# Optimization experiments

Measured on AMD Instinct MI355X. Metric: run time of the kernel, lower is better.

## Reference

```python
import jax, jax.numpy as jnp
import numpy as np

N_QUBITS = 14
N_LAYERS = 3
BATCH = 128


def _apply_1q(state, gate, w, n):
    """Apply a single-qubit gate on wire w (PennyLane wire 0 = most significant bit).
    state: (B, 2**n) complex. gate: (2,2) shared or (B,2,2) batched."""
    L, R = 2 ** w, 2 ** (n - 1 - w)
    s = state.reshape(-1, L, 2, R)
    if gate.ndim == 2:
        s = jnp.einsum('ij,aljr->alir', gate, s)
    else:
        s = jnp.einsum('aij,aljr->alir', gate, s)
    return s.reshape(state.shape)


def _apply_cnot(state, c, t, n):
    """CNOT with control wire c, target wire t on (B, 2**n) state."""
    s = state.reshape((-1,) + (2,) * n)
    ca = 1 + c
    s0 = jax.lax.index_in_dim(s, 0, ca, keepdims=False)
    s1 = jax.lax.index_in_dim(s, 1, ca, keepdims=False)
    # axis of target after removing control axis
    ta = 1 + t if t < c else t
    s1 = jnp.flip(s1, axis=ta)
    return jnp.stack([s0, s1], axis=ca).reshape(state.shape)


def _rx_gates(angles):
    """Batched RX gate matrices. angles: (B,) -> (B,2,2) complex64."""
    half = angles * 0.5
    c = jnp.cos(half).astype(jnp.complex64)
    s = (-1j) * jnp.sin(half).astype(jnp.complex64)
    return jnp.stack([jnp.stack([c, s], -1), jnp.stack([s, c], -1)], -2)


def _rot_gate(phi, theta, omega):
    """PennyLane Rot(phi,theta,omega) = RZ(omega) RY(theta) RZ(phi), (2,2) complex."""
    ct = jnp.cos(theta * 0.5).astype(jnp.complex64)
    st = jnp.sin(theta * 0.5).astype(jnp.complex64)
    ep = jnp.exp(-0.5j * (phi + omega))  # e^{-i(phi+omega)/2}
    em = jnp.exp(-0.5j * (phi - omega))  # e^{-i(phi-omega)/2}
    return jnp.stack([
        jnp.stack([ep * ct, -jnp.conj(em) * st]),
        jnp.stack([em * st, jnp.conj(ep) * ct]),
    ]).astype(jnp.complex64)


def _simulate(x, q_weights):
    B, n = x.shape
    state = jnp.zeros((B, 2 ** n), jnp.complex64).at[:, 0].set(1.0)
    # AngleEmbedding: RX(x_i) on wire i
    for w in range(n):
        state = _apply_1q(state, _rx_gates(x[:, w]), w, n)
    # StronglyEntanglingLayers: Rot on each wire, then ring of CNOTs with range r
    n_layers = q_weights.shape[0]
    for l in range(n_layers):
        for w in range(n):
            g = _rot_gate(q_weights[l, w, 0], q_weights[l, w, 1], q_weights[l, w, 2])
            state = _apply_1q(state, g, w, n)
        r = (l % (n - 1)) + 1  # PennyLane default ranges
        for w in range(n):
            state = _apply_cnot(state, w, (w + r) % n, n)
    return state


def _pauli_z_signs(n):
    idx = np.arange(2 ** n, dtype=np.int64)[:, None]
    shifts = np.arange(n - 1, -1, -1, dtype=np.int64)[None, :]  # wire 0 = MSB
    bits = (idx >> shifts) & 1
    return jnp.asarray(1.0 - 2.0 * bits, dtype=jnp.float32)  # (2**n, n)


def setup_inputs() -> dict:
    key = jax.random.key(0)
    k1, k2, k3, k4 = jax.random.split(key, 4)
    x = jax.random.normal(k1, (BATCH, N_QUBITS), dtype=jnp.float32)
    q_weights = jax.random.normal(k2, (N_LAYERS, N_QUBITS, 3), dtype=jnp.float32) * 0.01
    w_lin = jax.random.normal(k3, (1, N_QUBITS), dtype=jnp.float32) / np.sqrt(N_QUBITS)
    b_lin = jax.random.normal(k4, (1,), dtype=jnp.float32) * 0.01
    return {"x": x, "q_weights": q_weights, "w_lin": w_lin, "b_lin": b_lin}


def reference(x, q_weights, w_lin, b_lin):
    n = x.shape[1]
    state = _simulate(x, q_weights)
    probs = (state.real ** 2 + state.imag ** 2).astype(jnp.float32)  # (B, 2**n)
    expvals = probs @ _pauli_z_signs(n)  # (B, n) = <Z_i>
    logits = expvals @ w_lin.T + b_lin  # (B, 1)
    return logits
```

## Files before the change

kernel.cpp:

```cpp
#include <hip/hip_runtime.h>
#include <string.h>

#define NQ 14
#define NSTATE (1 << NQ)
#define NL 3
#define MAXP 12
#define BT 1024
#define NWAVES (BT / 64)

struct PassG {
    unsigned cmb8[16];
    unsigned R[10];
    unsigned gidx[4];
    unsigned nw;
    unsigned pad;
};
struct ParamsG {
    PassG pass[MAXP];
    unsigned ms[NQ];
    unsigned fmask[NQ];
    unsigned initIW[10];
};

struct C2x2 { float2 m[2][2]; };

__device__ __forceinline__ float2 cmul(float2 a, float2 b) {
    return make_float2(a.x * b.x - a.y * b.y, a.x * b.y + a.y * b.x);
}
__device__ __forceinline__ float2 cmac(float2 acc, float2 a, float2 b) {
    acc.x = fmaf(a.x, b.x, fmaf(-a.y, b.y, acc.x));
    acc.y = fmaf(a.x, b.y, fmaf(a.y, b.x, acc.y));
    return acc;
}

__device__ __forceinline__ C2x2 rot_gate(const float* qp) {
    float phi = qp[0], th = qp[1], om = qp[2];
    float ct, stt; __sincosf(0.5f * th, &stt, &ct);
    float sa, ca; __sincosf(0.5f * (phi + om), &sa, &ca);
    float sb, cb; __sincosf(0.5f * (phi - om), &sb, &cb);
    C2x2 G;
    G.m[0][0] = make_float2(ca * ct, -sa * ct);
    G.m[0][1] = make_float2(-cb * stt, -sb * stt);
    G.m[1][0] = make_float2(cb * stt, -sb * stt);
    G.m[1][1] = make_float2(ca * ct, sa * ct);
    return G;
}

__device__ __forceinline__ C2x2 fuse_rx(C2x2 G, float ang) {
    float sh, ch; __sincosf(0.5f * ang, &sh, &ch);
    float2 c = make_float2(ch, 0.f), is = make_float2(0.f, -sh);
    C2x2 R;
    #pragma unroll
    for (int i = 0; i < 2; ++i) {
        R.m[i][0] = cmac(cmul(G.m[i][0], c), G.m[i][1], is);
        R.m[i][1] = cmac(cmul(G.m[i][1], c), G.m[i][0], is);
    }
    return R;
}

__device__ __forceinline__ void load_pass(const PassG* __restrict__ p, int tid,
        unsigned cmb[16], unsigned gidx[4], unsigned& nw, unsigned& r)
{
    const uint4* c4 = (const uint4*)p->cmb8;
    uint4 u0 = c4[0], u1 = c4[1], u2 = c4[2], u3 = c4[3];
    cmb[0] = u0.x; cmb[1] = u0.y; cmb[2]  = u0.z; cmb[3]  = u0.w;
    cmb[4] = u1.x; cmb[5] = u1.y; cmb[6]  = u1.z; cmb[7]  = u1.w;
    cmb[8] = u2.x; cmb[9] = u2.y; cmb[10] = u2.z; cmb[11] = u2.w;
    cmb[12] = u3.x; cmb[13] = u3.y; cmb[14] = u3.z; cmb[15] = u3.w;
    unsigned rr = 0;
    #pragma unroll
    for (int j = 0; j < 10; ++j)
        rr ^= ((tid >> j) & 1) ? p->R[j] : 0u;
    r = rr;
    #pragma unroll
    for (int q = 0; q < 4; ++q) gidx[q] = p->gidx[q];
    nw = p->nw;
}

#define APPLY_STAGES()                                                      \
    {                                                                       \
        _Pragma("unroll")                                                   \
        for (int q = 0; q < 4; ++q) {                                       \
            if (q < (int)nwr) {                    \
                const int gi = (int)gidxr[q] * 4;                           \
                float2 g00 = gbuf[gi + 0], g01 = gbuf[gi + 1];              \
                float2 g10 = gbuf[gi + 2], g11 = gbuf[gi + 3];              \
                _Pragma("unroll")                                           \
                for (int i = 0; i < 16; ++i) {                              \
                    if (!((i >> q) & 1)) {                                  \
                        const int i1 = i | (1 << q);                        \
                        float2 a0 = a[i], a1 = a[i1];                       \
                        float2 n0 = cmac(cmul(g00, a0), g01, a1);           \
                        float2 n1 = cmac(cmul(g10, a0), g11, a1);           \
                        a[i] = n0; a[i1] = n1;                              \
                    }                                                       \
                }                                                           \
            }                                                               \
        }                                                                   \
    }

__global__ __launch_bounds__(BT) void qsim_kernel(
    const float* __restrict__ x, const float* __restrict__ qw,
    const float* __restrict__ wl, const float* __restrict__ bl,
    float* __restrict__ out, const ParamsG* __restrict__ pp, int np)
{
    __shared__ float2 st[NSTATE];
    __shared__ float2 gbuf[NL * NQ * 4];
    __shared__ float2 ubuf[NQ][2];
    __shared__ float red[NWAVES];

    const int tid = threadIdx.x;
    const int b = blockIdx.x;

    if (tid < NL * NQ) {
        int l = tid / NQ, w = tid % NQ;
        C2x2 G = rot_gate(qw + tid * 3);
        if (l == 0) {
            G = fuse_rx(G, x[b * NQ + w]);
            ubuf[w][0] = G.m[0][0];
            ubuf[w][1] = G.m[1][0];
        }
        gbuf[tid * 4 + 0] = G.m[0][0];
        gbuf[tid * 4 + 1] = G.m[0][1];
        gbuf[tid * 4 + 2] = G.m[1][0];
        gbuf[tid * 4 + 3] = G.m[1][1];
    }

    char* sb = (char*)st;
    float2 a[16];
    unsigned addr[16];
    unsigned cmbreg[16], gidxr[4], nwr, rn;

    load_pass(&pp->pass[0], tid, cmbreg, gidxr, nwr, rn);

    unsigned b0 = 0;
    #pragma unroll
    for (int j = 0; j < 10; ++j)
        b0 ^= ((tid >> j) & 1) ? pp->initIW[j] : 0u;

    __syncthreads();

    {
        const unsigned rb = rn << 3;
        float2 c = ubuf[0][b0 & 1];
        #pragma unroll
        for (int w = 1; w < 10; ++w)
            c = cmul(c, ubuf[w][(b0 >> w) & 1]);
        a[0] = cmul(c, ubuf[10][0]);
        a[1] = cmul(c, ubuf[10][1]);
        #pragma unroll
        for (int i = 0; i < 2; ++i) {
            a[2 + i] = cmul(a[i], ubuf[11][1]);
            a[i]     = cmul(a[i], ubuf[11][0]);
        }
        #pragma unroll
        for (int i = 0; i < 4; ++i) {
            a[4 + i] = cmul(a[i], ubuf[12][1]);
            a[i]     = cmul(a[i], ubuf[12][0]);
        }
        #pragma unroll
        for (int i = 0; i < 8; ++i) {
            a[8 + i] = cmul(a[i], ubuf[13][1]);
            a[i]     = cmul(a[i], ubuf[13][0]);
        }
        #pragma unroll
        for (int i = 0; i < 16; ++i)
            *(float2*)(sb + (rb ^ cmbreg[i])) = a[i];
    }

    load_pass(&pp->pass[1], tid, cmbreg, gidxr, nwr, rn);

    #pragma unroll 1
    for (int ps = 1; ps < np - 1; ++ps) {
        __syncthreads();
        const unsigned rb = rn << 3;
        #pragma unroll
        for (int i = 0; i < 16; ++i) addr[i] = rb ^ cmbreg[i];
        #pragma unroll
        for (int i = 0; i < 16; ++i)
            a[i] = *(const float2*)(sb + addr[i]);
        unsigned cmbn[16], gidxn[4], nwn, rnn;
        load_pass(&pp->pass[ps + 1], tid, cmbn, gidxn, nwn, rnn);
        APPLY_STAGES();
        #pragma unroll
        for (int i = 0; i < 16; ++i)
            *(float2*)(sb + addr[i]) = a[i];
        #pragma unroll
        for (int i = 0; i < 16; ++i) cmbreg[i] = cmbn[i];
        #pragma unroll
        for (int q = 0; q < 4; ++q) gidxr[q] = gidxn[q];
        nwr = nwn; rn = rnn;
    }

    float acc = 0.f;
    {
        __syncthreads();
        const unsigned rb = rn << 3;
        #pragma unroll
        for (int i = 0; i < 16; ++i) addr[i] = rb ^ cmbreg[i];
        #pragma unroll
        for (int i = 0; i < 16; ++i)
            a[i] = *(const float2*)(sb + addr[i]);
        APPLY_STAGES();

        float A[16];
        #pragma unroll
        for (int i = 0; i < 16; ++i) A[i] = 0.f;
        #pragma unroll
        for (int w = 0; w < NQ; ++w) {
            float v = wl[w];
            unsigned p0 = __popc(rn & pp->ms[w]) & 1u;
            float vs = p0 ? -v : v;
            const unsigned fm = pp->fmask[w];
            #pragma unroll
            for (int i = 0; i < 16; ++i)
                A[i] += ((fm >> i) & 1u) ? -vs : vs;
        }
        #pragma unroll
        for (int i = 0; i < 16; ++i)
            acc = fmaf(fmaf(a[i].x, a[i].x, a[i].y * a[i].y), A[i], acc);
    }

    #pragma unroll
    for (int off = 32; off > 0; off >>= 1) acc += __shfl_down(acc, off, 64);
    if ((tid & 63) == 0) red[tid >> 6] = acc;
    __syncthreads();
    if (tid == 0) {
        float s2 = 0.f;
        #pragma unroll
        for (int i = 0; i < NWAVES; ++i) s2 += red[i];
        out[b] = s2 + bl[0];
    }
}

struct GF2Basis {
    unsigned piv[NQ];
    GF2Basis() { for (int i = 0; i < NQ; ++i) piv[i] = 0; }
    bool insert(unsigned v) {
        for (int bb = NQ - 1; bb >= 0; --bb) {
            if (!((v >> bb) & 1)) continue;
            if (piv[bb]) v ^= piv[bb];
            else { piv[bb] = v; return true; }
        }
        return false;
    }
};

static inline int par16(unsigned v) { return __builtin_parity(v); }
static inline unsigned lcg_next(unsigned& s) { s = s * 1664525u + 1013904223u; return s >> 8; }

static unsigned gf_apply(const unsigned* C, unsigned v) {
    unsigned r = 0;
    while (v) { int j = __builtin_ctz(v); v &= v - 1; r ^= C[j]; }
    return r;
}

static bool gf_invert(const unsigned* C, unsigned* Ci) {
    unsigned rows[NQ], irows[NQ];
    for (int i = 0; i < NQ; ++i) {
        unsigned r = 0;
        for (int j = 0; j < NQ; ++j) r |= ((C[j] >> i) & 1u) << j;
        rows[i] = r; irows[i] = 1u << i;
    }
    for (int c = 0; c < NQ; ++c) {
        int p = -1;
        for (int r = c; r < NQ; ++r) if ((rows[r] >> c) & 1u) { p = r; break; }
        if (p < 0) return false;
        unsigned t = rows[p]; rows[p] = rows[c]; rows[c] = t;
        t = irows[p]; irows[p] = irows[c]; irows[c] = t;
        for (int r = 0; r < NQ; ++r)
            if (r != c && ((rows[r] >> c) & 1u)) { rows[r] ^= rows[c]; irows[r] ^= irows[c]; }
    }
    for (int j = 0; j < NQ; ++j) {
        unsigned col = 0;
        for (int i = 0; i < NQ; ++i) col |= ((irows[i] >> j) & 1u) << i;
        Ci[j] = col;
    }
    return true;
}

extern "C" void kernel_launch(void* const* d_in, const int* in_sizes, int n_in,
                              void* d_out, int out_size, void* d_ws, size_t ws_size,
                              hipStream_t stream) {
    const float* x  = (const float*)d_in[0];
    const float* qw = (const float*)d_in[1];
    const float* wl = (const float*)d_in[2];
    const float* bl = (const float*)d_in[3];
    float* out = (float*)d_out;

    const int B = in_sizes[0] / NQ;

    unsigned gs[NL * NQ], gm[NL * NQ];
    int ggi[NL * NQ];
    unsigned s[NQ], m[NQ], msIdx[NQ];
    for (int w = 0; w < NQ; ++w) s[w] = m[w] = 1u << (NQ - 1 - w);
    int ng = 0;
    for (int l = 0; l < NL; ++l) {
        if (l > 0) {
            for (int w = 0; w < NQ; ++w) {
                gs[ng] = s[w]; gm[ng] = m[w]; ggi[ng] = l * NQ + w; ++ng;
            }
        }
        int r = (l % (NQ - 1)) + 1;
        for (int w = 0; w < NQ; ++w) {
            int c = w, t = (w + r) % NQ;
            s[t] ^= s[c];
            m[c] ^= m[t];
        }
    }
    for (int w = 0; w < NQ; ++w) msIdx[w] = s[w];

    struct Raw { unsigned rv[10], cmb[16]; unsigned char gidx[4], nw; } raw[MAXP];

    {
        unsigned mm[4];
        for (int q = 0; q < 4; ++q) mm[q] = 1u << (3 - q);
        for (int j = 0; j < 10; ++j) raw[0].rv[j] = 1u << (13 - j);
        for (int idx = 0; idx < 16; ++idx) {
            unsigned c = 0;
            for (int q = 0; q < 4; ++q) if ((idx >> q) & 1) c ^= mm[q];
            raw[0].cmb[idx] = c;
        }
        for (int q = 0; q < 4; ++q) raw[0].gidx[q] = 0;
        raw[0].nw = 0;
    }

    bool used[NL * NQ] = {false};
    int np = 1, remaining = ng;
    while (remaining > 0 && np < MAXP) {
        unsigned pss[4], pmm[4];
        int pgi[4], nw = 0;
        GF2Basis gf;
        for (int g = 0; g < ng && nw < 4; ++g) {
            if (used[g]) continue;
            bool ok = true;
            for (int k = 0; k < nw && ok; ++k)
                if (par16(gs[g] & pmm[k]) || par16(pss[k] & gm[g])) ok = false;
            for (int h = 0; h < g && ok; ++h)
                if (!used[h] && (par16(gs[g] & gm[h]) || par16(gs[h] & gm[g]))) ok = false;
            if (!ok) continue;
            GF2Basis trial = gf;
            if (!trial.insert(gm[g])) continue;
            gf = trial;
            pss[nw] = gs[g]; pmm[nw] = gm[g]; pgi[nw] = g; ++nw;
            used[g] = true; --remaining;
        }
        unsigned mm[4], ss[4];
        for (int i = 0; i < nw; ++i) { mm[i] = pmm[i]; ss[i] = pss[i]; }
        for (int i = nw; i < 4; ++i) {
            unsigned cand = 0;
            for (int t = 0; t < NQ; ++t)
                if (gf.insert(1u << t)) { cand = 1u << t; break; }
            for (int j = 0; j < nw; ++j)
                if (par16(cand & ss[j])) cand ^= mm[j];
            mm[i] = cand; ss[i] = 0;
        }
        int nR = 0;
        for (int t = 0; t < NQ && nR < 10; ++t) {
            if (gf.insert(1u << t)) {
                unsigned v = 1u << t;
                for (int j = 0; j < nw; ++j)
                    if (par16(v & ss[j])) v ^= mm[j];
                raw[np].rv[nR++] = v;
            }
        }
        for (int idx = 0; idx < 16; ++idx) {
            unsigned c = 0;
            for (int q = 0; q < 4; ++q) if ((idx >> q) & 1) c ^= mm[q];
            raw[np].cmb[idx] = c;
        }
        for (int q = 0; q < 4; ++q)
            raw[np].gidx[q] = (unsigned char)(q < nw ? ggi[pgi[q]] : 0);
        raw[np].nw = (unsigned char)nw;
        ++np;
    }

    unsigned Cm[NQ], Ci[NQ];
    unsigned seed = 0x9E3779B9u;
    bool found = false;
    for (int tries = 0; tries < 5000 && !found; ++tries) {
        for (int j = 0; j < NQ; ++j) Cm[j] = lcg_next(seed) & (NSTATE - 1);
        if (!gf_invert(Cm, Ci)) continue;
        found = true;
        for (int p = 0; p < np && found; ++p) {
            unsigned piv[4] = {0, 0, 0, 0}; int npv = 0;
            for (int i = 0; i < 10; ++i) {
                unsigned w2 = gf_apply(Cm, raw[p].rv[i]);
                for (int bb = 0; bb < 4; ++bb)
                    if (((w2 >> bb) & 1u) && piv[bb]) w2 ^= piv[bb];
                if ((w2 & 15u) && npv < 4) { piv[__builtin_ctz(w2 & 15u)] = w2; ++npv; }
            }
            if (npv < 4) found = false;
        }
    }
    if (!found) {
        for (int j = 0; j < NQ; ++j) Cm[j] = 1u << j;
        gf_invert(Cm, Ci);
    }

    static ParamsG h_pg;
    memset(&h_pg, 0, sizeof(h_pg));
    for (int p = 0; p < np; ++p) {
        unsigned u[10];
        for (int i = 0; i < 10; ++i) u[i] = gf_apply(Cm, raw[p].rv[i]);
        unsigned piv[4] = {0, 0, 0, 0};
        int ord[10], npv = 0, rest[10], nrest = 0;
        for (int i = 0; i < 10; ++i) {
            unsigned w2 = u[i];
            for (int bb = 0; bb < 4; ++bb)
                if (((w2 >> bb) & 1u) && piv[bb]) w2 ^= piv[bb];
            if ((w2 & 15u) && npv < 4) { piv[__builtin_ctz(w2 & 15u)] = w2; ord[npv++] = i; }
            else rest[nrest++] = i;
        }
        int kk = 0;
        for (int i = 0; i < npv; ++i) h_pg.pass[p].R[kk++] = u[ord[i]];
        for (int i = 0; i < nrest; ++i) h_pg.pass[p].R[kk++] = u[rest[i]];
        for (int idx = 0; idx < 16; ++idx)
            h_pg.pass[p].cmb8[idx] = gf_apply(Cm, raw[p].cmb[idx]) << 3;
        for (int q = 0; q < 4; ++q) h_pg.pass[p].gidx[q] = raw[p].gidx[q];
        h_pg.pass[p].nw = raw[p].nw;
    }
    for (int w = 0; w < NQ; ++w) {
        unsigned msp = 0;
        for (int i = 0; i < NQ; ++i)
            msp |= (unsigned)(par16(Ci[i] & msIdx[w]) & 1) << i;
        h_pg.ms[w] = msp;
    }
    for (int w = 0; w < NQ; ++w) {
        unsigned fm = 0;
        for (int i = 0; i < 16; ++i)
            fm |= (unsigned)(par16((h_pg.pass[np - 1].cmb8[i] >> 3) & h_pg.ms[w]) & 1) << i;
        h_pg.fmask[w] = fm;
    }
    {
        unsigned tmask[NQ];
        for (int w = 0; w < NQ; ++w) {
            unsigned t = 0;
            for (int i = 0; i < NQ; ++i)
                t |= (unsigned)((Ci[i] >> (NQ - 1 - w)) & 1u) << i;
            tmask[w] = t;
        }
        for (int j = 0; j < 10; ++j) {
            unsigned iw = 0;
            for (int w = 0; w < NQ; ++w)
                iw |= (unsigned)(par16(h_pg.pass[0].R[j] & tmask[w]) & 1) << w;
            h_pg.initIW[j] = iw;
        }
    }

    ParamsG* d_pg = (ParamsG*)d_ws;
    hipMemcpyAsync(d_pg, &h_pg, sizeof(ParamsG), hipMemcpyHostToDevice, stream);
    qsim_kernel<<<dim3(B), dim3(BT), 0, stream>>>(x, qw, wl, bl, out, d_pg, np);
}
```

Measured before the change: 100.2 us.

## Pack extra gates along combined basis directions into each register pass

```diff
diff --git a/kernel.cpp b/kernel.cpp
--- a/kernel.cpp
+++ b/kernel.cpp
@@ -7,13 +7,17 @@
 #define MAXP 12
 #define BT 1024
 #define NWAVES (BT / 64)
+#define NEX 11
 
 struct PassG {
     unsigned cmb8[16];
     unsigned R[10];
     unsigned gidx[4];
     unsigned nw;
-    unsigned pad;
+    unsigned epm;
+    unsigned eg[11];
+    unsigned parw[11];
+    unsigned pad[2];
 };
 struct ParamsG {
     PassG pass[MAXP];
@@ -77,7 +81,32 @@
     nw = p->nw;
 }
 
-#define APPLY_STAGES()                                                      \
+template<int C>
+__device__ __forceinline__ void apply_extra(float2 a[16], const float2* gb,
+        unsigned w1, unsigned pw, unsigned rep)
+{
+    const unsigned sga = w1 & 0x3FFFu;
+    const int gi = (int)(w1 >> 16) * 4;
+    const unsigned og = __popc(rep & sga) & 1u;
+    const unsigned swv = pw ^ (og ? 0xFFFFu : 0u);
+    float2 g00 = gb[gi + 0], g01 = gb[gi + 1], g10 = gb[gi + 2], g11 = gb[gi + 3];
+    const int LB = C & (-C);
+    #pragma unroll
+    for (int i = 0; i < 16; ++i) {
+        if (!(i & LB)) {
+            const int i1 = i ^ C;
+            const bool sw = (swv >> i) & 1u;
+            float2 x0 = sw ? a[i1] : a[i];
+            float2 x1 = sw ? a[i]  : a[i1];
+            float2 n0 = cmac(cmul(g00, x0), g01, x1);
+            float2 n1 = cmac(cmul(g10, x0), g11, x1);
+            a[i]  = sw ? n1 : n0;
+            a[i1] = sw ? n0 : n1;
+        }
+    }
+}
+
+#define APPLY_BASIS()                                                       \
     {                                                                       \
         _Pragma("unroll")                                                   \
         for (int q = 0; q < 4; ++q) {                                       \
@@ -99,6 +128,23 @@
         }                                                                   \
     }
 
+#define APPLY_EXTRAS()                                                      \
+    {                                                                       \
+        if (epm) {                                                          \
+            if (epm & (1u<<0))  apply_extra<3> (a, gbuf, E0.x, E2.w, rn);   \
+            if (epm & (1u<<1))  apply_extra<5> (a, gbuf, E0.y, E3.x, rn);   \
+            if (epm & (1u<<2))  apply_extra<6> (a, gbuf, E0.z, E3.y, rn);   \
+            if (epm & (1u<<3))  apply_extra<9> (a, gbuf, E0.w, E3.z, rn);   \
+            if (epm & (1u<<4))  apply_extra<10>(a, gbuf, E1.x, E3.w, rn);   \
+            if (epm & (1u<<5))  apply_extra<12>(a, gbuf, E1.y, E4.x, rn);   \
+            if (epm & (1u<<6))  apply_extra<7> (a, gbuf, E1.z, E4.y, rn);   \
+            if (epm & (1u<<7))  apply_extra<11>(a, gbuf, E1.w, E4.z, rn);   \
+            if (epm & (1u<<8))  apply_extra<13>(a, gbuf, E2.x, E4.w, rn);   \
+            if (epm & (1u<<9))  apply_extra<14>(a, gbuf, E2.y, E5.x, rn);   \
+            if (epm & (1u<<10)) apply_extra<15>(a, gbuf, E2.z, E5.y, rn);   \
+        }                                                                   \
+    }
+
 __global__ __launch_bounds__(BT) void qsim_kernel(
     const float* __restrict__ x, const float* __restrict__ qw,
     const float* __restrict__ wl, const float* __restrict__ bl,
@@ -176,12 +222,16 @@
         const unsigned rb = rn << 3;
         #pragma unroll
         for (int i = 0; i < 16; ++i) addr[i] = rb ^ cmbreg[i];
+        const uint4* Eb = (const uint4*)((const char*)&pp->pass[ps] + 128);
+        uint4 E0 = Eb[0], E1 = Eb[1], E2 = Eb[2], E3 = Eb[3], E4 = Eb[4], E5 = Eb[5];
+        const unsigned epm = pp->pass[ps].epm;
         #pragma unroll
         for (int i = 0; i < 16; ++i)
             a[i] = *(const float2*)(sb + addr[i]);
         unsigned cmbn[16], gidxn[4], nwn, rnn;
         load_pass(&pp->pass[ps + 1], tid, cmbn, gidxn, nwn, rnn);
-        APPLY_STAGES();
+        APPLY_BASIS();
+        APPLY_EXTRAS();
         #pragma unroll
         for (int i = 0; i < 16; ++i)
             *(float2*)(sb + addr[i]) = a[i];
@@ -194,14 +244,19 @@
 
     float acc = 0.f;
     {
+        const int ps = np - 1;
         __syncthreads();
         const unsigned rb = rn << 3;
         #pragma unroll
         for (int i = 0; i < 16; ++i) addr[i] = rb ^ cmbreg[i];
+        const uint4* Eb = (const uint4*)((const char*)&pp->pass[ps] + 128);
+        uint4 E0 = Eb[0], E1 = Eb[1], E2 = Eb[2], E3 = Eb[3], E4 = Eb[4], E5 = Eb[5];
+        const unsigned epm = pp->pass[ps].epm;
         #pragma unroll
         for (int i = 0; i < 16; ++i)
             a[i] = *(const float2*)(sb + addr[i]);
-        APPLY_STAGES();
+        APPLY_BASIS();
+        APPLY_EXTRAS();
 
         float A[16];
         #pragma unroll
@@ -289,6 +344,10 @@
     float* out = (float*)d_out;
 
     const int B = in_sizes[0] / NQ;
+
+    static const int EXC[NEX] = {3, 5, 6, 9, 10, 12, 7, 11, 13, 14, 15};
+    int c2s[16]; for (int i = 0; i < 16; ++i) c2s[i] = -1;
+    for (int k = 0; k < NEX; ++k) c2s[EXC[k]] = k;
 
     unsigned gs[NL * NQ], gm[NL * NQ];
     int ggi[NL * NQ];
@@ -310,7 +369,15 @@
     }
     for (int w = 0; w < NQ; ++w) msIdx[w] = s[w];
 
-    struct Raw { unsigned rv[10], cmb[16]; unsigned char gidx[4], nw; } raw[MAXP];
+    struct Raw {
+        unsigned rv[10], cmb[16];
+        unsigned char gidx[4], nw;
+        int exgate[NEX];
+        unsigned exsel[NEX];
+        unsigned exT[NEX];
+    } raw[MAXP];
+    for (int p = 0; p < MAXP; ++p)
+        for (int k = 0; k < NEX; ++k) raw[p].exgate[k] = -1;
 
     {
         unsigned mm[4];
@@ -372,6 +439,48 @@
         for (int q = 0; q < 4; ++q)
             raw[np].gidx[q] = (unsigned char)(q < nw ? ggi[pgi[q]] : 0);
         raw[np].nw = (unsigned char)nw;
+
+        {
+            int exCirc[NEX]; int nExtra = 0;
+            for (int g = 0; g < ng; ++g) {
+                if (used[g]) continue;
+                int c = -1;
+                for (int t2 = 3; t2 < 16; ++t2) {
+                    if (__builtin_popcount((unsigned)t2) < 2) continue;
+                    unsigned xr = 0;
+                    for (int j = 0; j < 4; ++j) if ((t2 >> j) & 1) xr ^= mm[j];
+                    if (xr == gm[g]) { c = t2; break; }
+                }
+                if (c < 0) continue;
+                int slot = c2s[c];
+                if (slot < 0 || raw[np].exgate[slot] >= 0) continue;
+                unsigned T = 0;
+                for (int j = 0; j < 4; ++j)
+                    T |= (unsigned)(par16(mm[j] & gs[g]) & 1) << j;
+                {
+                    int sp = 0;
+                    for (int j = 0; j < 4; ++j) if ((c >> j) & 1) sp ^= (T >> j) & 1;
+                    if (!sp) continue;
+                }
+                bool ok = true;
+                for (int e = 0; e < nExtra && ok; ++e) {
+                    int h = exCirc[e];
+                    if (par16(gs[g] & gm[h]) || par16(gs[h] & gm[g])) ok = false;
+                }
+                for (int kk = 0; kk < nw && ok; ++kk) {
+                    int h = pgi[kk];
+                    if (h > g && (par16(gs[g] & gm[h]) || par16(gs[h] & gm[g]))) ok = false;
+                }
+                for (int h = 0; h < g && ok; ++h)
+                    if (!used[h] && (par16(gs[g] & gm[h]) || par16(gs[h] & gm[g]))) ok = false;
+                if (!ok) continue;
+                raw[np].exgate[slot] = ggi[g];
+                raw[np].exsel[slot] = gs[g];
+                raw[np].exT[slot] = T;
+                exCirc[nExtra++] = g;
+                used[g] = true; --remaining;
+            }
+        }
         ++np;
     }
 
@@ -419,6 +528,20 @@
             h_pg.pass[p].cmb8[idx] = gf_apply(Cm, raw[p].cmb[idx]) << 3;
         for (int q = 0; q < 4; ++q) h_pg.pass[p].gidx[q] = raw[p].gidx[q];
         h_pg.pass[p].nw = raw[p].nw;
+        unsigned epm = 0;
+        for (int k = 0; k < NEX; ++k) {
+            if (raw[p].exgate[k] < 0) continue;
+            epm |= 1u << k;
+            unsigned sga = 0;
+            for (int i = 0; i < NQ; ++i)
+                sga |= (unsigned)(par16(Ci[i] & raw[p].exsel[k]) & 1) << i;
+            h_pg.pass[p].eg[k] = sga | ((unsigned)raw[p].exgate[k] << 16);
+            unsigned T = raw[p].exT[k], pw = 0;
+            for (int i = 0; i < 16; ++i)
+                pw |= (unsigned)(__builtin_popcount(i & T) & 1) << i;
+            h_pg.pass[p].parw[k] = pw;
+        }
+        h_pg.pass[p].epm = epm;
     }
     for (int w = 0; w < NQ; ++w) {
         unsigned msp = 0;
```

Result: slower. 102.7 us (+2.6%).
